# Performance work log

Measured on AMD Instinct MI355X. Metric: run time of the kernel, lower is better.

Reference implementation:

```python
import jax, jax.numpy as jnp
import numpy as np

B, H, W_IMG, C = 256, 88, 88, 3
NUM_CH = 64
MATCH_ATOL = 0.0


def setup_inputs() -> dict:
    key = jax.random.key(0)
    k1, k2 = jax.random.split(key)
    rgb = jax.random.randint(k1, (B, H, W_IMG, C), 0, 256, dtype=jnp.int32)
    # conv params: HWIO layout for lax.conv_general_dilated
    Wc = jax.random.normal(k2, (8, 8, C, NUM_CH), dtype=jnp.float32) * 0.05
    bc = jnp.zeros((NUM_CH,), dtype=jnp.float32)
    return {"rgb": rgb, "Wc": Wc, "bc": bc}


def _guidance_from_feats(out):
    # out: [B, 121, 64]
    # pairwise feature-equality counts (O(N^2) broadcast, as in original)
    eq = jnp.max(jnp.abs(out[:, None, :, :] - out[:, :, None, :]), axis=-1) <= MATCH_ATOL
    counts = jnp.sum(eq, axis=-1)  # [B, 121] int32, always >= 1 (self-match)
    M = counts.shape[-1]
    hist = jax.vmap(lambda c: jnp.bincount(c, length=M + 1))(counts)  # [B, M+1]
    cum = jnp.cumsum(hist, axis=-1)
    K = int(0.3 * M)
    allow_freq = cum <= K
    kmin = jnp.min(counts, axis=-1)  # [B]
    allow_freq = jnp.logical_or(allow_freq, jnp.arange(M + 1)[None, :] == kmin[:, None])
    # gather allow flag per position via its count value
    mask_keep = jnp.take_along_axis(allow_freq[:, None, :], counts[..., None], axis=-1)[..., 0]
    fcounts = counts.astype(jnp.float32)
    logits = jnp.where(mask_keep, -jnp.log(fcounts), -jnp.inf)
    attn = jax.nn.softmax(logits, axis=-1)  # [B, 121]
    guidance = attn.reshape(attn.shape[0], 1, 11, 11)
    return jax.lax.stop_gradient(guidance)


def reference(rgb, Wc, bc):
    x = rgb.astype(jnp.float32) / 255.0  # [B, 88, 88, 3]
    feats = jax.lax.conv_general_dilated(
        x, Wc, window_strides=(8, 8), padding='VALID',
        dimension_numbers=('NHWC', 'HWIO', 'NHWC')) + bc
    feats = jax.nn.relu(feats)  # [B, 11, 11, 64]
    vis_op = feats.reshape(feats.shape[0], -1, feats.shape[-1])  # [B, 121, 64]
    guidance = _guidance_from_feats(vis_op)  # [B, 1, 11, 11]
    return (vis_op, guidance)
```

## Files before the change

kernel.cpp:

```cpp
#include <hip/hip_runtime.h>
#include <hip/hip_bf16.h>

#define B_SZ 256
#define NCH 64
#define NPOS 121
#define NPATCH (B_SZ * NPOS)
#define KTOT 192
#define MTILE 64
#define NBLK (NPATCH / MTILE)
#define LDK 200

typedef short bf16x8 __attribute__((ext_vector_type(8)));
typedef float f32x4 __attribute__((ext_vector_type(4)));

static __device__ inline unsigned f2bf(float x) {
  union { float f; unsigned u; } a; a.f = x;
  unsigned r = a.u + 0x7FFFu + ((a.u >> 16) & 1u);
  return r >> 16;
}
static __device__ inline unsigned pack2(float lo, float hi) {
  return f2bf(lo) | (f2bf(hi) << 16);
}

__global__ __launch_bounds__(256) void conv_mfma(
    const int* __restrict__ rgb, const float* __restrict__ Wc,
    const float* __restrict__ bc, float* __restrict__ out) {
  __shared__ __align__(16) unsigned short A[MTILE * LDK];
  __shared__ __align__(16) unsigned short Bt[NCH * LDK];
  const int tid = threadIdx.x;
  const int blk = blockIdx.x;

  for (int s = tid; s < 512; s += 256) {
    const int pl = s >> 3, ky = s & 7;
    const int P = blk * MTILE + pl;
    const int b = P / NPOS;
    const int r = P - b * NPOS;
    const int oy = r / 11;
    const int ox = r - oy * 11;
    const int4* s4 = (const int4*)(rgb + (((b * 88 + oy * 8 + ky) * 88) + ox * 8) * 3);
    float v[24];
    #pragma unroll
    for (int q = 0; q < 6; ++q) {
      const int4 t = s4[q];
      v[q * 4 + 0] = (float)t.x * (1.f / 255.f);
      v[q * 4 + 1] = (float)t.y * (1.f / 255.f);
      v[q * 4 + 2] = (float)t.z * (1.f / 255.f);
      v[q * 4 + 3] = (float)t.w * (1.f / 255.f);
    }
    unsigned short* dst = &A[pl * LDK + ky * 24];
    #pragma unroll
    for (int q = 0; q < 3; ++q) {
      uint4 p;
      p.x = pack2(v[q * 8 + 0], v[q * 8 + 1]);
      p.y = pack2(v[q * 8 + 2], v[q * 8 + 3]);
      p.z = pack2(v[q * 8 + 4], v[q * 8 + 5]);
      p.w = pack2(v[q * 8 + 6], v[q * 8 + 7]);
      *(uint4*)(dst + q * 8) = p;
    }
  }

  {
    const int n = tid & 63;
    const int kg = tid >> 6;
    #pragma unroll
    for (int q = 0; q < 6; ++q) {
      const int k0 = kg * 48 + q * 8;
      float w[8];
      #pragma unroll
      for (int j = 0; j < 8; ++j) w[j] = Wc[(k0 + j) * NCH + n];
      uint4 p;
      p.x = pack2(w[0], w[1]); p.y = pack2(w[2], w[3]);
      p.z = pack2(w[4], w[5]); p.w = pack2(w[6], w[7]);
      *(uint4*)&Bt[n * LDK + k0] = p;
    }
  }
  __syncthreads();

  const int lane = tid & 63;
  const int w = tid >> 6;
  const int m0 = (w >> 1) * 32;
  const int n0 = (w & 1) * 32;
  const int lr = lane & 15;
  const int lg = lane >> 4;

  f32x4 acc[2][2] = {};
  #pragma unroll
  for (int ks = 0; ks < 6; ++ks) {
    const int k0 = ks * 32 + lg * 8;
    const bf16x8 a0 = *(const bf16x8*)&A[(m0 + lr) * LDK + k0];
    const bf16x8 a1 = *(const bf16x8*)&A[(m0 + 16 + lr) * LDK + k0];
    const bf16x8 b0 = *(const bf16x8*)&Bt[(n0 + lr) * LDK + k0];
    const bf16x8 b1 = *(const bf16x8*)&Bt[(n0 + 16 + lr) * LDK + k0];
    acc[0][0] = __builtin_amdgcn_mfma_f32_16x16x32_bf16(a0, b0, acc[0][0], 0, 0, 0);
    acc[0][1] = __builtin_amdgcn_mfma_f32_16x16x32_bf16(a0, b1, acc[0][1], 0, 0, 0);
    acc[1][0] = __builtin_amdgcn_mfma_f32_16x16x32_bf16(a1, b0, acc[1][0], 0, 0, 0);
    acc[1][1] = __builtin_amdgcn_mfma_f32_16x16x32_bf16(a1, b1, acc[1][1], 0, 0, 0);
  }

  #pragma unroll
  for (int ni = 0; ni < 2; ++ni) {
    const int col = n0 + ni * 16 + lr;
    const float bias = bc[col];
    #pragma unroll
    for (int mi = 0; mi < 2; ++mi) {
      #pragma unroll
      for (int rr = 0; rr < 4; ++rr) {
        const int row = m0 + mi * 16 + lg * 4 + rr;
        out[(size_t)(blk * MTILE + row) * NCH + col] = fmaxf(acc[mi][ni][rr] + bias, 0.f);
      }
    }
  }
}

__global__ __launch_bounds__(256) void guide_kernel(
    const float* __restrict__ feats, float* __restrict__ gout) {
  const int b = blockIdx.x, tid = threadIdx.x;
  __shared__ __align__(16) unsigned f[NPOS * NCH];
  __shared__ unsigned sig[NPOS];
  __shared__ int counts[NPOS];
  __shared__ int allow[NPOS + 1];
  __shared__ float wsum[4];

  if (tid < NPOS) sig[tid] = 0u;
  if (tid <= NPOS) allow[tid] = 0;
  __syncthreads();

  const uint4* src = (const uint4*)(feats + (size_t)b * NPOS * NCH);
  for (int g = tid; g < NPOS * 16; g += 256) {
    const uint4 v = src[g];
    ((uint4*)f)[g] = v;
    const int row = g >> 4;
    const int k = (g & 15) * 4;
    unsigned h = 0;
    h ^= (v.x ^ (v.x >> 15)) * ((2u * (k + 0) + 1u) * 0x9E3779B9u);
    h ^= (v.y ^ (v.y >> 15)) * ((2u * (k + 1) + 1u) * 0x9E3779B9u);
    h ^= (v.z ^ (v.z >> 15)) * ((2u * (k + 2) + 1u) * 0x9E3779B9u);
    h ^= (v.w ^ (v.w >> 15)) * ((2u * (k + 3) + 1u) * 0x9E3779B9u);
    atomicXor(&sig[row], h);
  }
  __syncthreads();

  if (tid < NPOS) {
    const unsigned si = sig[tid];
    int m = 0;
    for (int j = 0; j < NPOS; ++j) m += (sig[j] == si) ? 1 : 0;
    int cnt = 1;
    if (m > 1) {
      cnt = 0;
      for (int j = 0; j < NPOS; ++j) {
        if (sig[j] == si) {
          int eq = 1;
          for (int c = 0; c < NCH; ++c) eq &= (f[tid * NCH + c] == f[j * NCH + c]);
          cnt += eq;
        }
      }
    }
    counts[tid] = cnt;
    atomicAdd(&allow[cnt], 1);
  }
  __syncthreads();

  if (tid == 0) {
    int kmin = counts[0];
    for (int i = 1; i < NPOS; ++i) kmin = min(kmin, counts[i]);
    int cum = 0;
    const int K = 36;
    for (int k = 0; k <= NPOS; ++k) {
      cum += allow[k];
      allow[k] = (cum <= K || k == kmin) ? 1 : 0;
    }
  }
  __syncthreads();

  float wv = 0.f;
  if (tid < NPOS) {
    const int c = counts[tid];
    if (allow[c]) wv = 1.f / (float)c;
  }
  float s = wv;
  #pragma unroll
  for (int off = 1; off < 64; off <<= 1) s += __shfl_xor(s, off, 64);
  if ((tid & 63) == 0) wsum[tid >> 6] = s;
  __syncthreads();
  const float Z = wsum[0] + wsum[1] + wsum[2] + wsum[3];
  if (tid < NPOS) gout[(size_t)b * NPOS + tid] = wv / Z;
}

extern "C" void kernel_launch(void* const* d_in, const int* in_sizes, int n_in,
                              void* d_out, int out_size, void* d_ws, size_t ws_size,
                              hipStream_t stream) {
  const int*   rgb = (const int*)d_in[0];
  const float* Wc  = (const float*)d_in[1];
  const float* bc  = (const float*)d_in[2];
  float* out   = (float*)d_out;
  float* guide = out + (size_t)NPATCH * NCH;

  conv_mfma<<<NBLK, 256, 0, stream>>>(rgb, Wc, bc, out);
  guide_kernel<<<B_SZ, 256, 0, stream>>>(out, guide);
}
```

Before: 86.20 us.

## Fuse conv and guidance into one per-image kernel with prepacked weights

Replaces the two-kernel pipeline with a weight prepack kernel plus one fused kernel per image. That kernel stages the whole image as bf16 in shared memory, runs the MFMA conv with weights held in registers, and computes the guidance directly from features kept in LDS. This removes the global round trip of the features between kernels and the per-tile weight repacking. The serial histogram/cumsum step becomes a per-thread count-compare, and the kmin search becomes a wave reduction. In exchange there are only 256 blocks, heavy LDS use (about 46KB) and high register pressure, which may lower occupancy.

```diff
diff --git a/kernel.cpp b/kernel.cpp
--- a/kernel.cpp
+++ b/kernel.cpp
@@ -6,183 +6,185 @@
 #define NPOS 121
 #define NPATCH (B_SZ * NPOS)
 #define KTOT 192
-#define MTILE 64
-#define NBLK (NPATCH / MTILE)
-#define LDK 200
+#define RGB_W 264
+#define LDR 264
+#define FST 68
 
 typedef short bf16x8 __attribute__((ext_vector_type(8)));
 typedef float f32x4 __attribute__((ext_vector_type(4)));
 
 static __device__ inline unsigned f2bf(float x) {
   union { float f; unsigned u; } a; a.f = x;
-  unsigned r = a.u + 0x7FFFu + ((a.u >> 16) & 1u);
-  return r >> 16;
+  return (a.u + 0x7FFFu + ((a.u >> 16) & 1u)) >> 16;
 }
 static __device__ inline unsigned pack2(float lo, float hi) {
   return f2bf(lo) | (f2bf(hi) << 16);
 }
 
-__global__ __launch_bounds__(256) void conv_mfma(
-    const int* __restrict__ rgb, const float* __restrict__ Wc,
-    const float* __restrict__ bc, float* __restrict__ out) {
-  __shared__ __align__(16) unsigned short A[MTILE * LDK];
-  __shared__ __align__(16) unsigned short Bt[NCH * LDK];
-  const int tid = threadIdx.x;
-  const int blk = blockIdx.x;
-
-  for (int s = tid; s < 512; s += 256) {
-    const int pl = s >> 3, ky = s & 7;
-    const int P = blk * MTILE + pl;
-    const int b = P / NPOS;
-    const int r = P - b * NPOS;
-    const int oy = r / 11;
-    const int ox = r - oy * 11;
-    const int4* s4 = (const int4*)(rgb + (((b * 88 + oy * 8 + ky) * 88) + ox * 8) * 3);
-    float v[24];
-    #pragma unroll
-    for (int q = 0; q < 6; ++q) {
-      const int4 t = s4[q];
-      v[q * 4 + 0] = (float)t.x * (1.f / 255.f);
-      v[q * 4 + 1] = (float)t.y * (1.f / 255.f);
-      v[q * 4 + 2] = (float)t.z * (1.f / 255.f);
-      v[q * 4 + 3] = (float)t.w * (1.f / 255.f);
-    }
-    unsigned short* dst = &A[pl * LDK + ky * 24];
-    #pragma unroll
-    for (int q = 0; q < 3; ++q) {
-      uint4 p;
-      p.x = pack2(v[q * 8 + 0], v[q * 8 + 1]);
-      p.y = pack2(v[q * 8 + 2], v[q * 8 + 3]);
-      p.z = pack2(v[q * 8 + 4], v[q * 8 + 5]);
-      p.w = pack2(v[q * 8 + 6], v[q * 8 + 7]);
-      *(uint4*)(dst + q * 8) = p;
-    }
-  }
-
+__global__ __launch_bounds__(256) void pack_b(const float* __restrict__ Wc,
+                                              unsigned short* __restrict__ Btg) {
+  const int n = threadIdx.x & 63;
+  const int q = threadIdx.x >> 6;
+  const int k0 = q * 48;
+  float w[48];
+  #pragma unroll
+  for (int j = 0; j < 48; ++j) w[j] = Wc[(k0 + j) * NCH + n];
+  #pragma unroll
+  for (int c = 0; c < 6; ++c) {
+    uint4 p;
+    p.x = pack2(w[c*8+0], w[c*8+1]); p.y = pack2(w[c*8+2], w[c*8+3]);
+    p.z = pack2(w[c*8+4], w[c*8+5]); p.w = pack2(w[c*8+6], w[c*8+7]);
+    *(uint4*)&Btg[n * KTOT + k0 + c * 8] = p;
+  }
+}
+
+__global__ __launch_bounds__(256) void fused(
+    const int* __restrict__ rgb, const unsigned short* __restrict__ Btg,
+    const float* __restrict__ bc, float* __restrict__ out,
+    float* __restrict__ gout) {
+  __shared__ __align__(16) unsigned short rgbL[88 * LDR];
+  __shared__ unsigned sig[NPOS];
+  __shared__ int counts[NPOS];
+  __shared__ int redi[4];
+  __shared__ float redf[4];
+  unsigned* fbits = (unsigned*)rgbL;
+
+  const int b = blockIdx.x, tid = threadIdx.x;
+  const int lane = tid & 63, w = tid >> 6;
+  const int lr = lane & 15, lg = lane >> 4;
+
+  bf16x8 bfr[4][6];
+  #pragma unroll
+  for (int ni = 0; ni < 4; ++ni)
+    #pragma unroll
+    for (int ks = 0; ks < 6; ++ks)
+      bfr[ni][ks] = *(const bf16x8*)&Btg[(ni * 16 + lr) * KTOT + ks * 32 + lg * 8];
+
+  const int4* src4 = (const int4*)(rgb + (size_t)b * 88 * RGB_W);
+  #pragma unroll 4
+  for (int it = 0; it < 22; ++it) {
+    const int i = tid + it * 256;
+    const int4 t = src4[i];
+    const int e = i * 4, row = e / RGB_W, col = e - row * RGB_W;
+    uint2 p;
+    p.x = pack2((float)t.x * (1.f/255.f), (float)t.y * (1.f/255.f));
+    p.y = pack2((float)t.z * (1.f/255.f), (float)t.w * (1.f/255.f));
+    *(uint2*)&rgbL[row * LDR + col] = p;
+  }
   {
-    const int n = tid & 63;
-    const int kg = tid >> 6;
-    #pragma unroll
-    for (int q = 0; q < 6; ++q) {
-      const int k0 = kg * 48 + q * 8;
-      float w[8];
-      #pragma unroll
-      for (int j = 0; j < 8; ++j) w[j] = Wc[(k0 + j) * NCH + n];
-      uint4 p;
-      p.x = pack2(w[0], w[1]); p.y = pack2(w[2], w[3]);
-      p.z = pack2(w[4], w[5]); p.w = pack2(w[6], w[7]);
-      *(uint4*)&Bt[n * LDK + k0] = p;
-    }
-  }
-  __syncthreads();
-
-  const int lane = tid & 63;
-  const int w = tid >> 6;
-  const int m0 = (w >> 1) * 32;
-  const int n0 = (w & 1) * 32;
-  const int lr = lane & 15;
-  const int lg = lane >> 4;
-
-  f32x4 acc[2][2] = {};
+    const int i = tid + 5632;
+    if (i < 5808) {
+      const int4 t = src4[i];
+      const int e = i * 4, row = e / RGB_W, col = e - row * RGB_W;
+      uint2 p;
+      p.x = pack2((float)t.x * (1.f/255.f), (float)t.y * (1.f/255.f));
+      p.y = pack2((float)t.z * (1.f/255.f), (float)t.w * (1.f/255.f));
+      *(uint2*)&rgbL[row * LDR + col] = p;
+    }
+  }
+  __syncthreads();
+
+  const int m0 = w * 32;
+  f32x4 acc[2][4] = {};
+  int kyv[6], kmv[6];
   #pragma unroll
   for (int ks = 0; ks < 6; ++ks) {
     const int k0 = ks * 32 + lg * 8;
-    const bf16x8 a0 = *(const bf16x8*)&A[(m0 + lr) * LDK + k0];
-    const bf16x8 a1 = *(const bf16x8*)&A[(m0 + 16 + lr) * LDK + k0];
-    const bf16x8 b0 = *(const bf16x8*)&Bt[(n0 + lr) * LDK + k0];
-    const bf16x8 b1 = *(const bf16x8*)&Bt[(n0 + 16 + lr) * LDK + k0];
-    acc[0][0] = __builtin_amdgcn_mfma_f32_16x16x32_bf16(a0, b0, acc[0][0], 0, 0, 0);
-    acc[0][1] = __builtin_amdgcn_mfma_f32_16x16x32_bf16(a0, b1, acc[0][1], 0, 0, 0);
-    acc[1][0] = __builtin_amdgcn_mfma_f32_16x16x32_bf16(a1, b0, acc[1][0], 0, 0, 0);
-    acc[1][1] = __builtin_amdgcn_mfma_f32_16x16x32_bf16(a1, b1, acc[1][1], 0, 0, 0);
-  }
-
-  #pragma unroll
-  for (int ni = 0; ni < 2; ++ni) {
-    const int col = n0 + ni * 16 + lr;
-    const float bias = bc[col];
-    #pragma unroll
-    for (int mi = 0; mi < 2; ++mi) {
+    kyv[ks] = k0 / 24; kmv[ks] = k0 - kyv[ks] * 24;
+  }
+  #pragma unroll
+  for (int mi = 0; mi < 2; ++mi) {
+    const int p = m0 + mi * 16 + lr;
+    const int pe = p > 120 ? 120 : p;
+    const int oy = pe / 11, ox = pe - oy * 11;
+    #pragma unroll
+    for (int ks = 0; ks < 6; ++ks) {
+      const bf16x8 a =
+          *(const bf16x8*)&rgbL[(oy * 8 + kyv[ks]) * LDR + ox * 24 + kmv[ks]];
       #pragma unroll
-      for (int rr = 0; rr < 4; ++rr) {
-        const int row = m0 + mi * 16 + lg * 4 + rr;
-        out[(size_t)(blk * MTILE + row) * NCH + col] = fmaxf(acc[mi][ni][rr] + bias, 0.f);
+      for (int ni = 0; ni < 4; ++ni)
+        acc[mi][ni] = __builtin_amdgcn_mfma_f32_16x16x32_bf16(
+            a, bfr[ni][ks], acc[mi][ni], 0, 0, 0);
+    }
+  }
+  __syncthreads();
+
+  float bias[4];
+  #pragma unroll
+  for (int ni = 0; ni < 4; ++ni) bias[ni] = bc[ni * 16 + lr];
+  float* outB = out + (size_t)b * NPOS * NCH;
+  #pragma unroll
+  for (int mi = 0; mi < 2; ++mi) {
+    #pragma unroll
+    for (int rr = 0; rr < 4; ++rr) {
+      const int p = m0 + mi * 16 + lg * 4 + rr;
+      if (p < NPOS) {
+        #pragma unroll
+        for (int ni = 0; ni < 4; ++ni) {
+          const int col = ni * 16 + lr;
+          const float v = fmaxf(acc[mi][ni][rr] + bias[ni], 0.f) + 0.f;
+          outB[p * NCH + col] = v;
+          fbits[p * FST + col] = __float_as_uint(v);
+        }
       }
     }
   }
-}
-
-__global__ __launch_bounds__(256) void guide_kernel(
-    const float* __restrict__ feats, float* __restrict__ gout) {
-  const int b = blockIdx.x, tid = threadIdx.x;
-  __shared__ __align__(16) unsigned f[NPOS * NCH];
-  __shared__ unsigned sig[NPOS];
-  __shared__ int counts[NPOS];
-  __shared__ int allow[NPOS + 1];
-  __shared__ float wsum[4];
-
-  if (tid < NPOS) sig[tid] = 0u;
-  if (tid <= NPOS) allow[tid] = 0;
-  __syncthreads();
-
-  const uint4* src = (const uint4*)(feats + (size_t)b * NPOS * NCH);
-  for (int g = tid; g < NPOS * 16; g += 256) {
-    const uint4 v = src[g];
-    ((uint4*)f)[g] = v;
-    const int row = g >> 4;
-    const int k = (g & 15) * 4;
+  __syncthreads();
+
+  if (tid < NPOS) {
+    const uint4* fr = (const uint4*)&fbits[tid * FST];
     unsigned h = 0;
-    h ^= (v.x ^ (v.x >> 15)) * ((2u * (k + 0) + 1u) * 0x9E3779B9u);
-    h ^= (v.y ^ (v.y >> 15)) * ((2u * (k + 1) + 1u) * 0x9E3779B9u);
-    h ^= (v.z ^ (v.z >> 15)) * ((2u * (k + 2) + 1u) * 0x9E3779B9u);
-    h ^= (v.w ^ (v.w >> 15)) * ((2u * (k + 3) + 1u) * 0x9E3779B9u);
-    atomicXor(&sig[row], h);
-  }
-  __syncthreads();
-
+    #pragma unroll
+    for (int q = 0; q < 16; ++q) {
+      const uint4 v = fr[q];
+      h ^= (v.x ^ (v.x >> 15)) * ((8u*q + 1u) * 0x9E3779B9u);
+      h ^= (v.y ^ (v.y >> 15)) * ((8u*q + 3u) * 0x9E3779B9u);
+      h ^= (v.z ^ (v.z >> 15)) * ((8u*q + 5u) * 0x9E3779B9u);
+      h ^= (v.w ^ (v.w >> 15)) * ((8u*q + 7u) * 0x9E3779B9u);
+    }
+    sig[tid] = h;
+  }
+  __syncthreads();
+
+  int cnt = 0x7fffffff;
   if (tid < NPOS) {
     const unsigned si = sig[tid];
     int m = 0;
     for (int j = 0; j < NPOS; ++j) m += (sig[j] == si) ? 1 : 0;
-    int cnt = 1;
+    cnt = 1;
     if (m > 1) {
       cnt = 0;
       for (int j = 0; j < NPOS; ++j) {
         if (sig[j] == si) {
           int eq = 1;
-          for (int c = 0; c < NCH; ++c) eq &= (f[tid * NCH + c] == f[j * NCH + c]);
+          for (int c = 0; c < NCH; ++c) eq &= (fbits[tid*FST + c] == fbits[j*FST + c]);
           cnt += eq;
         }
       }
     }
     counts[tid] = cnt;
-    atomicAdd(&allow[cnt], 1);
-  }
-  __syncthreads();
-
-  if (tid == 0) {
-    int kmin = counts[0];
-    for (int i = 1; i < NPOS; ++i) kmin = min(kmin, counts[i]);
-    int cum = 0;
-    const int K = 36;
-    for (int k = 0; k <= NPOS; ++k) {
-      cum += allow[k];
-      allow[k] = (cum <= K || k == kmin) ? 1 : 0;
-    }
-  }
-  __syncthreads();
+  }
+  __syncthreads();
+
+  int km_ = cnt;
+  #pragma unroll
+  for (int off = 1; off < 64; off <<= 1) km_ = min(km_, __shfl_xor(km_, off, 64));
+  if (lane == 0) redi[w] = km_;
+  __syncthreads();
+  const int kmin = min(min(redi[0], redi[1]), min(redi[2], redi[3]));
 
   float wv = 0.f;
   if (tid < NPOS) {
-    const int c = counts[tid];
-    if (allow[c]) wv = 1.f / (float)c;
+    int cum = 0;
+    for (int j = 0; j < NPOS; ++j) cum += (counts[j] <= cnt) ? 1 : 0;
+    if (cum <= 36 || cnt == kmin) wv = 1.f / (float)cnt;
   }
   float s = wv;
   #pragma unroll
   for (int off = 1; off < 64; off <<= 1) s += __shfl_xor(s, off, 64);
-  if ((tid & 63) == 0) wsum[tid >> 6] = s;
-  __syncthreads();
-  const float Z = wsum[0] + wsum[1] + wsum[2] + wsum[3];
+  if (lane == 0) redf[w] = s;
+  __syncthreads();
+  const float Z = redf[0] + redf[1] + redf[2] + redf[3];
   if (tid < NPOS) gout[(size_t)b * NPOS + tid] = wv / Z;
 }
 
@@ -194,7 +196,8 @@
   const float* bc  = (const float*)d_in[2];
   float* out   = (float*)d_out;
   float* guide = out + (size_t)NPATCH * NCH;
-
-  conv_mfma<<<NBLK, 256, 0, stream>>>(rgb, Wc, bc, out);
-  guide_kernel<<<B_SZ, 256, 0, stream>>>(out, guide);
-}
+  unsigned short* Btg = (unsigned short*)d_ws;
+
+  pack_b<<<1, 256, 0, stream>>>(Wc, Btg);
+  fused<<<B_SZ, 256, 0, stream>>>(rgb, Btg, bc, out, guide);
+}
```

Result: faster. 84.17 us (-2.4%).
